# Kernel tuning notes

Hardware: AMD Instinct MI355X
Metric: run time of the kernel (lower is better)

The kernel has to match this reference:

```python
import jax, jax.numpy as jnp
import numpy as np

QK_DIM = 64
V_DIM = 64
NUM_Q_HEADS = 16
NUM_KV_HEADS = 4
GROUP = NUM_Q_HEADS // NUM_KV_HEADS
SCALE = 1.0 / (QK_DIM ** 0.5)


def setup_inputs() -> dict:
    key = jax.random.key(0)
    kq, kk, kv = jax.random.split(key, 3)
    B, S = 2, 2048
    Q = jax.random.normal(kq, (B, S, NUM_Q_HEADS * QK_DIM), dtype=jnp.float32)
    K = jax.random.normal(kk, (B, S, NUM_KV_HEADS * QK_DIM), dtype=jnp.float32)
    V = jax.random.normal(kv, (B, S, NUM_KV_HEADS * V_DIM), dtype=jnp.float32)
    # causal mask, [B, 1, S, S]; 0 entries are masked (matches masked_fill(mask == 0, -inf))
    mask = jnp.broadcast_to(jnp.tril(jnp.ones((S, S), dtype=jnp.int32))[None, None], (B, 1, S, S))
    return {"Q": Q, "K": K, "V": V, "mask": mask}


def reference(Q, K, V, mask):
    B, S, _ = Q.shape
    # [B, Hkv, g, S, d]
    Qg = Q.reshape(B, S, NUM_Q_HEADS, QK_DIM).transpose(0, 2, 1, 3).reshape(B, NUM_KV_HEADS, GROUP, S, QK_DIM)
    Kh = K.reshape(B, S, NUM_KV_HEADS, QK_DIM).transpose(0, 2, 1, 3)  # [B, Hkv, S, d]
    Vh = V.reshape(B, S, NUM_KV_HEADS, V_DIM).transpose(0, 2, 1, 3)   # [B, Hkv, S, dv]
    # scores: [B, Hkv, g, S, S]
    scores = jnp.einsum('bhgsd,bhtd->bhgst', Qg, Kh) * SCALE
    scores = jnp.where(mask[:, None] == 0, -jnp.inf, scores)
    probs = jax.nn.softmax(scores, axis=-1)
    # dropout p=0.0 -> identity (eval semantics)
    out = jnp.einsum('bhgst,bhtv->bhgsv', probs, Vh)
    return out
```

## Files before the change

### kernel.cpp

```cpp
#include <hip/hip_runtime.h>
#include <hip/hip_bf16.h>

typedef unsigned short u16;
typedef unsigned int u32;
typedef __attribute__((ext_vector_type(8))) short bf16x8;
typedef __attribute__((ext_vector_type(4))) float f32x4;

#define S_LEN 2048
#define NHQ   16
#define NHKV  4
#define HD    64
#define KVBLK 64
#define PPAD  72
#define KVSTR (NHKV*HD)
#define QSTR  (NHQ*HD)
#define TILE_U16 4096
#define HEAD_U16 (32*TILE_U16)
#define VT_OFF   (8*HEAD_U16)
#define QSCALE 0.18033688011112042f
#define DEFER_THR 8.0f

__device__ __forceinline__ u32 cvt2(float lo, float hi) {
    __hip_bfloat162 hh = __float22bfloat162_rn(make_float2(lo, hi));
    union { __hip_bfloat162 h; u32 u; } c; c.h = hh; return c.u;
}
__device__ __forceinline__ u16 cvt1(float x) {
    __hip_bfloat16 hh = __float2bfloat16(x);
    union { __hip_bfloat16 h; u16 u; } c; c.h = hh; return c.u;
}

typedef __attribute__((address_space(3))) u32 lds_u32;
typedef __attribute__((address_space(1))) const u32 glb_u32;
__device__ __forceinline__ void gld_lds16(const void* g, void* l) {
    __builtin_amdgcn_global_load_lds((glb_u32*)g, (lds_u32*)l, 16, 0, 0);
}

__global__ __launch_bounds__(256)
void prep_kv(const float* __restrict__ Kp, const float* __restrict__ Vp,
             u16* __restrict__ WS)
{
    const int bid = blockIdx.x;
    const int t   = bid & 31;
    const int kvh = (bid >> 5) & 3;
    const int b   = bid >> 7;
    const int tid = threadIdx.x;

    u16* kt = WS + (size_t)bid * TILE_U16;
    u16* vt = WS + VT_OFF + (size_t)bid * TILE_U16;

    {
        const int r   = tid >> 2;
        const int c16 = (tid & 3) << 4;
        const float* kg = Kp + ((size_t)(b*S_LEN) + t*64 + r) * KVSTR + kvh*HD + c16;
        const float4 a  = *(const float4*)(kg);
        const float4 b4 = *(const float4*)(kg + 4);
        const float4 c  = *(const float4*)(kg + 8);
        const float4 d  = *(const float4*)(kg + 12);
        const int swz = (r & 7) << 3;
        *(uint4*)(kt + r*64 + (c16 ^ swz)) =
            make_uint4(cvt2(a.x,a.y), cvt2(a.z,a.w), cvt2(b4.x,b4.y), cvt2(b4.z,b4.w));
        *(uint4*)(kt + r*64 + ((c16+8) ^ swz)) =
            make_uint4(cvt2(c.x,c.y), cvt2(c.z,c.w), cvt2(d.x,d.y), cvt2(d.z,d.w));
    }
    {
        const int kv  = tid & 63;
        const int dv0 = (tid >> 6) << 4;
        const float* vg = Vp + ((size_t)(b*S_LEN) + t*64 + kv) * KVSTR + kvh*HD + dv0;
        float4 vv[4];
        vv[0] = *(const float4*)(vg);
        vv[1] = *(const float4*)(vg + 4);
        vv[2] = *(const float4*)(vg + 8);
        vv[3] = *(const float4*)(vg + 12);
        #pragma unroll
        for (int g4 = 0; g4 < 4; ++g4) {
            const int dv = dv0 + g4*4;
            vt[(dv+0)*64 + (kv ^ (((dv+0)&7)<<3))] = cvt1(vv[g4].x);
            vt[(dv+1)*64 + (kv ^ (((dv+1)&7)<<3))] = cvt1(vv[g4].y);
            vt[(dv+2)*64 + (kv ^ (((dv+2)&7)<<3))] = cvt1(vv[g4].z);
            vt[(dv+3)*64 + (kv ^ (((dv+3)&7)<<3))] = cvt1(vv[g4].w);
        }
    }
}

__global__ __launch_bounds__(256, 3)
void gqa_fwd_kernel(const float* __restrict__ Qp, const u16* __restrict__ WS,
                    float* __restrict__ Op)
{
    __shared__ __align__(16) u16 Kl[2][TILE_U16];
    __shared__ __align__(16) u16 Vl[2][TILE_U16];
    __shared__ __align__(16) u16 Pl[4][16][PPAD];

    const int tid  = threadIdx.x;
    const int w    = tid >> 6;
    const int lane = tid & 63;
    const int l16  = lane & 15;
    const int quad = lane >> 4;

    const int bid  = blockIdx.x;
    const int head = bid & 31;
    const int qt   = 31 - (bid >> 5);
    const int kvh  = head & 3;
    const int b    = (head >> 2) & 1;
    const int qh   = kvh * 4 + (head >> 3);

    const u16* Kt = WS + (size_t)(b*4 + kvh) * HEAD_U16;
    const u16* Vt = WS + VT_OFF + (size_t)(b*4 + kvh) * HEAD_U16;

    const int relq = w*16 + l16;
    const int qrow = qt*64 + relq;
    const float* qp = Qp + ((size_t)b * S_LEN + qrow) * QSTR + qh*HD;
    float*       ob = Op + ((size_t)(b*NHQ + qh) * S_LEN + qrow) * HD;

    const size_t gofs = (size_t)w*2048 + (size_t)lane*16;

    const int rswz = (l16 & 7) << 3;

    {
        const char* kg = (const char*)Kt + gofs;
        const char* vg = (const char*)Vt + gofs;
        char* kl = (char*)(&Kl[0][0]) + w*2048;
        char* vl = (char*)(&Vl[0][0]) + w*2048;
        gld_lds16(kg, kl);  gld_lds16(kg + 1024, kl + 1024);
        gld_lds16(vg, vl);  gld_lds16(vg + 1024, vl + 1024);
    }

    bf16x8 qf[2];
    #pragma unroll
    for (int kk = 0; kk < 2; ++kk) {
        const float4 x = *(const float4*)(qp + kk*32 + quad*8);
        const float4 y = *(const float4*)(qp + kk*32 + quad*8 + 4);
        union { u32 u[4]; bf16x8 v; } t4;
        t4.u[0] = cvt2(x.x*QSCALE, x.y*QSCALE);
        t4.u[1] = cvt2(x.z*QSCALE, x.w*QSCALE);
        t4.u[2] = cvt2(y.x*QSCALE, y.y*QSCALE);
        t4.u[3] = cvt2(y.z*QSCALE, y.w*QSCALE);
        qf[kk] = t4.v;
    }

    f32x4 oacc[4];
    #pragma unroll
    for (int nb = 0; nb < 4; ++nb) { oacc[nb][0]=0.f; oacc[nb][1]=0.f; oacc[nb][2]=0.f; oacc[nb][3]=0.f; }
    float m_s = -1e30f;
    float l_p = 0.f;

    __syncthreads();

    for (int t = 0; t <= qt; ++t) {
        const int bf = t & 1;
        if (t < qt) {
            const char* kg = (const char*)(Kt + (size_t)(t+1)*TILE_U16) + gofs;
            const char* vg = (const char*)(Vt + (size_t)(t+1)*TILE_U16) + gofs;
            char* kl = (char*)(&Kl[bf^1][0]) + w*2048;
            char* vl = (char*)(&Vl[bf^1][0]) + w*2048;
            gld_lds16(kg, kl);  gld_lds16(kg + 1024, kl + 1024);
            gld_lds16(vg, vl);  gld_lds16(vg + 1024, vl + 1024);
        }

        f32x4 s[4];
        __builtin_amdgcn_s_setprio(1);
        #pragma unroll
        for (int nb = 0; nb < 4; ++nb) {
            f32x4 acc = {0.f,0.f,0.f,0.f};
            #pragma unroll
            for (int kk = 0; kk < 2; ++kk) {
                bf16x8 kf = *(const bf16x8*)(&Kl[bf][(nb*16 + l16)*64 + ((kk*32 + quad*8) ^ rswz)]);
                acc = __builtin_amdgcn_mfma_f32_16x16x32_bf16(kf, qf[kk], acc, 0, 0, 0);
            }
            s[nb] = acc;
        }
        __builtin_amdgcn_s_setprio(0);

        if (t == qt) {
            #pragma unroll
            for (int nb = 0; nb < 4; ++nb)
                #pragma unroll
                for (int r = 0; r < 4; ++r)
                    if (nb*16 + quad*4 + r > relq) s[nb][r] = -1e30f;
        }

        float a0 = fmaxf(fmaxf(s[0][0], s[0][1]), fmaxf(s[0][2], s[0][3]));
        float a1 = fmaxf(fmaxf(s[1][0], s[1][1]), fmaxf(s[1][2], s[1][3]));
        float a2 = fmaxf(fmaxf(s[2][0], s[2][1]), fmaxf(s[2][2], s[2][3]));
        float a3 = fmaxf(fmaxf(s[3][0], s[3][1]), fmaxf(s[3][2], s[3][3]));
        const float lmax = fmaxf(fmaxf(a0, a1), fmaxf(a2, a3));

        if (!__all(lmax <= m_s + DEFER_THR)) {
            float rmax = fmaxf(lmax, __shfl_xor(lmax, 16));
            rmax = fmaxf(rmax, __shfl_xor(rmax, 32));
            const float mnew = fmaxf(m_s, rmax);
            const float cf   = __builtin_amdgcn_exp2f(m_s - mnew);
            m_s = mnew;
            l_p *= cf;
            #pragma unroll
            for (int nb = 0; nb < 4; ++nb)
                #pragma unroll
                for (int r = 0; r < 4; ++r) oacc[nb][r] *= cf;
        }

        float ps[4];
        #pragma unroll
        for (int nb = 0; nb < 4; ++nb) {
            const float p0 = __builtin_amdgcn_exp2f(s[nb][0] - m_s);
            const float p1 = __builtin_amdgcn_exp2f(s[nb][1] - m_s);
            const float p2 = __builtin_amdgcn_exp2f(s[nb][2] - m_s);
            const float p3 = __builtin_amdgcn_exp2f(s[nb][3] - m_s);
            s[nb][0]=p0; s[nb][1]=p1; s[nb][2]=p2; s[nb][3]=p3;
            ps[nb] = (p0 + p1) + (p2 + p3);
        }
        l_p += (ps[0] + ps[1]) + (ps[2] + ps[3]);

        #pragma unroll
        for (int nb = 0; nb < 4; ++nb)
            *(uint2*)(&Pl[w][l16][nb*16 + quad*4]) =
                make_uint2(cvt2(s[nb][0], s[nb][1]), cvt2(s[nb][2], s[nb][3]));
        bf16x8 pfrag[2];
        #pragma unroll
        for (int kk = 0; kk < 2; ++kk)
            pfrag[kk] = *(const bf16x8*)(&Pl[w][l16][kk*32 + quad*8]);

        __builtin_amdgcn_s_setprio(1);
        #pragma unroll
        for (int nb = 0; nb < 4; ++nb) {
            #pragma unroll
            for (int kk = 0; kk < 2; ++kk) {
                bf16x8 vf = *(const bf16x8*)(&Vl[bf][(nb*16 + l16)*64 + ((kk*32 + quad*8) ^ rswz)]);
                oacc[nb] = __builtin_amdgcn_mfma_f32_16x16x32_bf16(vf, pfrag[kk], oacc[nb], 0, 0, 0);
            }
        }
        __builtin_amdgcn_s_setprio(0);

        __syncthreads();
    }

    l_p += __shfl_xor(l_p, 16);
    l_p += __shfl_xor(l_p, 32);
    const float inv = 1.0f / l_p;
    #pragma unroll
    for (int nb = 0; nb < 4; ++nb) {
        float4 o4;
        o4.x = oacc[nb][0] * inv;
        o4.y = oacc[nb][1] * inv;
        o4.z = oacc[nb][2] * inv;
        o4.w = oacc[nb][3] * inv;
        *(float4*)(ob + nb*16 + quad*4) = o4;
    }
}

extern "C" void kernel_launch(void* const* d_in, const int* in_sizes, int n_in,
                              void* d_out, int out_size, void* d_ws, size_t ws_size,
                              hipStream_t stream) {
    const float* Q = (const float*)d_in[0];
    const float* K = (const float*)d_in[1];
    const float* V = (const float*)d_in[2];
    float* O  = (float*)d_out;
    u16*  WS = (u16*)d_ws;

    prep_kv<<<dim3(256), dim3(256), 0, stream>>>(K, V, WS);
    gqa_fwd_kernel<<<dim3(1024), dim3(256), 0, stream>>>(Q, WS, O);
}
```

Baseline: 46.19 us.

## Switch attention to 32x32x16 MFMA with register-only P via permlane32 swap

The attention kernel now uses 32x32x16 bf16 MFMA instructions, with each wave owning 32 query rows, so a block is two waves of 128 threads instead of four. The P tile is rearranged into the B-operand layout in registers using v_permlane32_swap, which drops the LDS write/read round trip and its shared buffer. The larger MFMA shape cuts K/V fragment reloads per query row and instruction count. In exchange each wave needs more accumulator registers and blocks have fewer waves, which may lower occupancy and latency hiding.

```diff
diff --git a/kernel.cpp b/kernel.cpp
--- a/kernel.cpp
+++ b/kernel.cpp
@@ -4,14 +4,12 @@
 typedef unsigned short u16;
 typedef unsigned int u32;
 typedef __attribute__((ext_vector_type(8))) short bf16x8;
-typedef __attribute__((ext_vector_type(4))) float f32x4;
+typedef __attribute__((ext_vector_type(16))) float f32x16;
 
 #define S_LEN 2048
 #define NHQ   16
 #define NHKV  4
 #define HD    64
-#define KVBLK 64
-#define PPAD  72
 #define KVSTR (NHKV*HD)
 #define QSTR  (NHQ*HD)
 #define TILE_U16 4096
@@ -82,19 +80,18 @@
     }
 }
 
-__global__ __launch_bounds__(256, 3)
+__global__ __launch_bounds__(128, 2)
 void gqa_fwd_kernel(const float* __restrict__ Qp, const u16* __restrict__ WS,
                     float* __restrict__ Op)
 {
     __shared__ __align__(16) u16 Kl[2][TILE_U16];
     __shared__ __align__(16) u16 Vl[2][TILE_U16];
-    __shared__ __align__(16) u16 Pl[4][16][PPAD];
 
     const int tid  = threadIdx.x;
     const int w    = tid >> 6;
     const int lane = tid & 63;
-    const int l16  = lane & 15;
-    const int quad = lane >> 4;
+    const int q31  = lane & 31;
+    const int h    = lane >> 5;
 
     const int bid  = blockIdx.x;
     const int head = bid & 31;
@@ -106,40 +103,43 @@
     const u16* Kt = WS + (size_t)(b*4 + kvh) * HEAD_U16;
     const u16* Vt = WS + VT_OFF + (size_t)(b*4 + kvh) * HEAD_U16;
 
-    const int relq = w*16 + l16;
-    const int qrow = qt*64 + relq;
+    const int qrow = qt*64 + w*32 + q31;
     const float* qp = Qp + ((size_t)b * S_LEN + qrow) * QSTR + qh*HD;
     float*       ob = Op + ((size_t)(b*NHQ + qh) * S_LEN + qrow) * HD;
 
-    const size_t gofs = (size_t)w*2048 + (size_t)lane*16;
-
-    const int rswz = (l16 & 7) << 3;
+    const size_t gofs = (size_t)w*1024 + (size_t)lane*16;
+    const int    lofs = w*1024;
+
+    const int rswz = (q31 & 7) << 3;
+    const int qcmp = q31 + 32*w;
 
     {
         const char* kg = (const char*)Kt + gofs;
         const char* vg = (const char*)Vt + gofs;
-        char* kl = (char*)(&Kl[0][0]) + w*2048;
-        char* vl = (char*)(&Vl[0][0]) + w*2048;
-        gld_lds16(kg, kl);  gld_lds16(kg + 1024, kl + 1024);
-        gld_lds16(vg, vl);  gld_lds16(vg + 1024, vl + 1024);
-    }
-
-    bf16x8 qf[2];
+        #pragma unroll
+        for (int r = 0; r < 4; ++r) {
+            gld_lds16(kg + r*2048, (char*)(&Kl[0][0]) + lofs + r*2048);
+            gld_lds16(vg + r*2048, (char*)(&Vl[0][0]) + lofs + r*2048);
+        }
+    }
+
+    bf16x8 qf[4];
     #pragma unroll
-    for (int kk = 0; kk < 2; ++kk) {
-        const float4 x = *(const float4*)(qp + kk*32 + quad*8);
-        const float4 y = *(const float4*)(qp + kk*32 + quad*8 + 4);
+    for (int ks = 0; ks < 4; ++ks) {
+        const int d = ks*16 + h*8;
+        const float4 x = *(const float4*)(qp + d);
+        const float4 y = *(const float4*)(qp + d + 4);
         union { u32 u[4]; bf16x8 v; } t4;
         t4.u[0] = cvt2(x.x*QSCALE, x.y*QSCALE);
         t4.u[1] = cvt2(x.z*QSCALE, x.w*QSCALE);
         t4.u[2] = cvt2(y.x*QSCALE, y.y*QSCALE);
         t4.u[3] = cvt2(y.z*QSCALE, y.w*QSCALE);
-        qf[kk] = t4.v;
-    }
-
-    f32x4 oacc[4];
+        qf[ks] = t4.v;
+    }
+
+    f32x16 oacc0, oacc1;
     #pragma unroll
-    for (int nb = 0; nb < 4; ++nb) { oacc[nb][0]=0.f; oacc[nb][1]=0.f; oacc[nb][2]=0.f; oacc[nb][3]=0.f; }
+    for (int i = 0; i < 16; ++i) { oacc0[i] = 0.f; oacc1[i] = 0.f; }
     float m_s = -1e30f;
     float l_p = 0.f;
 
@@ -150,99 +150,103 @@
         if (t < qt) {
             const char* kg = (const char*)(Kt + (size_t)(t+1)*TILE_U16) + gofs;
             const char* vg = (const char*)(Vt + (size_t)(t+1)*TILE_U16) + gofs;
-            char* kl = (char*)(&Kl[bf^1][0]) + w*2048;
-            char* vl = (char*)(&Vl[bf^1][0]) + w*2048;
-            gld_lds16(kg, kl);  gld_lds16(kg + 1024, kl + 1024);
-            gld_lds16(vg, vl);  gld_lds16(vg + 1024, vl + 1024);
-        }
-
-        f32x4 s[4];
+            #pragma unroll
+            for (int r = 0; r < 4; ++r) {
+                gld_lds16(kg + r*2048, (char*)(&Kl[bf^1][0]) + lofs + r*2048);
+                gld_lds16(vg + r*2048, (char*)(&Vl[bf^1][0]) + lofs + r*2048);
+            }
+        }
+
+        f32x16 s0, s1;
+        #pragma unroll
+        for (int i = 0; i < 16; ++i) { s0[i] = 0.f; s1[i] = 0.f; }
         __builtin_amdgcn_s_setprio(1);
         #pragma unroll
-        for (int nb = 0; nb < 4; ++nb) {
-            f32x4 acc = {0.f,0.f,0.f,0.f};
-            #pragma unroll
-            for (int kk = 0; kk < 2; ++kk) {
-                bf16x8 kf = *(const bf16x8*)(&Kl[bf][(nb*16 + l16)*64 + ((kk*32 + quad*8) ^ rswz)]);
-                acc = __builtin_amdgcn_mfma_f32_16x16x32_bf16(kf, qf[kk], acc, 0, 0, 0);
-            }
-            s[nb] = acc;
+        for (int ks = 0; ks < 4; ++ks) {
+            const int col = (ks*16 + h*8) ^ rswz;
+            bf16x8 k0 = *(const bf16x8*)(&Kl[bf][q31*64 + col]);
+            bf16x8 k1 = *(const bf16x8*)(&Kl[bf][(32 + q31)*64 + col]);
+            s0 = __builtin_amdgcn_mfma_f32_32x32x16_bf16(k0, qf[ks], s0, 0, 0, 0);
+            s1 = __builtin_amdgcn_mfma_f32_32x32x16_bf16(k1, qf[ks], s1, 0, 0, 0);
         }
         __builtin_amdgcn_s_setprio(0);
 
         if (t == qt) {
             #pragma unroll
-            for (int nb = 0; nb < 4; ++nb)
-                #pragma unroll
-                for (int r = 0; r < 4; ++r)
-                    if (nb*16 + quad*4 + r > relq) s[nb][r] = -1e30f;
-        }
-
-        float a0 = fmaxf(fmaxf(s[0][0], s[0][1]), fmaxf(s[0][2], s[0][3]));
-        float a1 = fmaxf(fmaxf(s[1][0], s[1][1]), fmaxf(s[1][2], s[1][3]));
-        float a2 = fmaxf(fmaxf(s[2][0], s[2][1]), fmaxf(s[2][2], s[2][3]));
-        float a3 = fmaxf(fmaxf(s[3][0], s[3][1]), fmaxf(s[3][2], s[3][3]));
-        const float lmax = fmaxf(fmaxf(a0, a1), fmaxf(a2, a3));
+            for (int rg = 0; rg < 16; ++rg) {
+                const int kvl = (rg & 3) + 8*(rg >> 2) + 4*h;
+                if (kvl > qcmp)      s0[rg] = -1e30f;
+                if (kvl + 32 > qcmp) s1[rg] = -1e30f;
+            }
+        }
+
+        float mx[8];
+        #pragma unroll
+        for (int i = 0; i < 8; ++i)
+            mx[i] = fmaxf(fmaxf(s0[i], s0[i+8]), fmaxf(s1[i], s1[i+8]));
+        const float lmax = fmaxf(fmaxf(fmaxf(mx[0],mx[1]), fmaxf(mx[2],mx[3])),
+                                 fmaxf(fmaxf(mx[4],mx[5]), fmaxf(mx[6],mx[7])));
 
         if (!__all(lmax <= m_s + DEFER_THR)) {
-            float rmax = fmaxf(lmax, __shfl_xor(lmax, 16));
-            rmax = fmaxf(rmax, __shfl_xor(rmax, 32));
+            float rmax = fmaxf(lmax, __shfl_xor(lmax, 32));
             const float mnew = fmaxf(m_s, rmax);
             const float cf   = __builtin_amdgcn_exp2f(m_s - mnew);
             m_s = mnew;
             l_p *= cf;
             #pragma unroll
-            for (int nb = 0; nb < 4; ++nb)
-                #pragma unroll
-                for (int r = 0; r < 4; ++r) oacc[nb][r] *= cf;
-        }
-
-        float ps[4];
-        #pragma unroll
-        for (int nb = 0; nb < 4; ++nb) {
-            const float p0 = __builtin_amdgcn_exp2f(s[nb][0] - m_s);
-            const float p1 = __builtin_amdgcn_exp2f(s[nb][1] - m_s);
-            const float p2 = __builtin_amdgcn_exp2f(s[nb][2] - m_s);
-            const float p3 = __builtin_amdgcn_exp2f(s[nb][3] - m_s);
-            s[nb][0]=p0; s[nb][1]=p1; s[nb][2]=p2; s[nb][3]=p3;
-            ps[nb] = (p0 + p1) + (p2 + p3);
-        }
-        l_p += (ps[0] + ps[1]) + (ps[2] + ps[3]);
-
-        #pragma unroll
-        for (int nb = 0; nb < 4; ++nb)
-            *(uint2*)(&Pl[w][l16][nb*16 + quad*4]) =
-                make_uint2(cvt2(s[nb][0], s[nb][1]), cvt2(s[nb][2], s[nb][3]));
-        bf16x8 pfrag[2];
-        #pragma unroll
-        for (int kk = 0; kk < 2; ++kk)
-            pfrag[kk] = *(const bf16x8*)(&Pl[w][l16][kk*32 + quad*8]);
+            for (int i = 0; i < 16; ++i) { oacc0[i] *= cf; oacc1[i] *= cf; }
+        }
+
+        float ps0 = 0.f, ps1 = 0.f;
+        #pragma unroll
+        for (int rg = 0; rg < 16; ++rg) {
+            const float p0 = __builtin_amdgcn_exp2f(s0[rg] - m_s);
+            const float p1 = __builtin_amdgcn_exp2f(s1[rg] - m_s);
+            s0[rg] = p0; ps0 += p0;
+            s1[rg] = p1; ps1 += p1;
+        }
+        l_p += ps0 + ps1;
+
+        u32 Aw[8], Bw[8];
+        #pragma unroll
+        for (int m = 0; m < 4; ++m) {
+            Aw[m]   = cvt2(s0[m*4+0], s0[m*4+1]);
+            Bw[m]   = cvt2(s0[m*4+2], s0[m*4+3]);
+            Aw[4+m] = cvt2(s1[m*4+0], s1[m*4+1]);
+            Bw[4+m] = cvt2(s1[m*4+2], s1[m*4+3]);
+        }
 
         __builtin_amdgcn_s_setprio(1);
         #pragma unroll
-        for (int nb = 0; nb < 4; ++nb) {
-            #pragma unroll
-            for (int kk = 0; kk < 2; ++kk) {
-                bf16x8 vf = *(const bf16x8*)(&Vl[bf][(nb*16 + l16)*64 + ((kk*32 + quad*8) ^ rswz)]);
-                oacc[nb] = __builtin_amdgcn_mfma_f32_16x16x32_bf16(vf, pfrag[kk], oacc[nb], 0, 0, 0);
-            }
+        for (int c = 0; c < 4; ++c) {
+            u32 w0 = Aw[2*c], w2 = Aw[2*c+1];
+            u32 w1 = Bw[2*c], w3 = Bw[2*c+1];
+            asm("v_permlane32_swap_b32 %0, %1" : "+v"(w0), "+v"(w2));
+            asm("v_permlane32_swap_b32 %0, %1" : "+v"(w1), "+v"(w3));
+            union { u32 u[4]; bf16x8 v; } pu;
+            pu.u[0] = w0; pu.u[1] = w1; pu.u[2] = w2; pu.u[3] = w3;
+            const int col = (c*16 + h*8) ^ rswz;
+            bf16x8 v0 = *(const bf16x8*)(&Vl[bf][q31*64 + col]);
+            bf16x8 v1 = *(const bf16x8*)(&Vl[bf][(32 + q31)*64 + col]);
+            oacc0 = __builtin_amdgcn_mfma_f32_32x32x16_bf16(v0, pu.v, oacc0, 0, 0, 0);
+            oacc1 = __builtin_amdgcn_mfma_f32_32x32x16_bf16(v1, pu.v, oacc1, 0, 0, 0);
         }
         __builtin_amdgcn_s_setprio(0);
 
         __syncthreads();
     }
 
-    l_p += __shfl_xor(l_p, 16);
     l_p += __shfl_xor(l_p, 32);
     const float inv = 1.0f / l_p;
     #pragma unroll
-    for (int nb = 0; nb < 4; ++nb) {
-        float4 o4;
-        o4.x = oacc[nb][0] * inv;
-        o4.y = oacc[nb][1] * inv;
-        o4.z = oacc[nb][2] * inv;
-        o4.w = oacc[nb][3] * inv;
-        *(float4*)(ob + nb*16 + quad*4) = o4;
+    for (int k = 0; k < 4; ++k) {
+        float4 o;
+        o.x = oacc0[4*k+0]*inv; o.y = oacc0[4*k+1]*inv;
+        o.z = oacc0[4*k+2]*inv; o.w = oacc0[4*k+3]*inv;
+        *(float4*)(ob + 8*k + 4*h) = o;
+        o.x = oacc1[4*k+0]*inv; o.y = oacc1[4*k+1]*inv;
+        o.z = oacc1[4*k+2]*inv; o.w = oacc1[4*k+3]*inv;
+        *(float4*)(ob + 32 + 8*k + 4*h) = o;
     }
 }
 
@@ -256,5 +260,5 @@
     u16*  WS = (u16*)d_ws;
 
     prep_kv<<<dim3(256), dim3(256), 0, stream>>>(K, V, WS);
-    gqa_fwd_kernel<<<dim3(1024), dim3(256), 0, stream>>>(Q, WS, O);
-}
+    gqa_fwd_kernel<<<dim3(1024), dim3(128), 0, stream>>>(Q, WS, O);
+}
```

Measured after the change: 56.71 us. 1.23x slower.
